# Kernel optimization log

Hardware: AMD Instinct MI355X
Metric: run time of the kernel (lower is better)

## Reference

```python
import jax, jax.numpy as jnp
import numpy as np

B, S, D, H, W1, G = 2, 4096, 768, 12, 256, 8  # W1 = one-sided window (attention_window // 2)
HD = D // H
NC = S // W1  # number of query chunks of size W1
NEG = -1e9


def setup_inputs():
    key = jax.random.key(0)
    ks = jax.random.split(key, 9)
    def w(k):
        return jax.random.normal(k, (D, D), jnp.float32) * 0.02
    zb = jnp.zeros((D,), jnp.float32)
    # mask: >0 global, 0 local, <0 masked. First G tokens are global.
    mask = jnp.zeros((B, 1, 1, S), jnp.int32).at[:, :, :, :G].set(1)
    return {
        "hidden_states": jax.random.normal(ks[0], (B, S, D), jnp.float32),
        "attention_mask": mask,
        "Wq": w(ks[1]), "bq": zb,
        "Wk": w(ks[2]), "bk": zb,
        "Wv": w(ks[3]), "bv": zb,
        "Wqg": w(ks[4]), "bqg": zb,
        "Wkg": w(ks[5]), "bkg": zb,
        "Wvg": w(ks[6]), "bvg": zb,
        "Wo": w(ks[7]), "bo": zb,
        "n_global": G,
    }


def reference(hidden_states, attention_mask, Wq, bq, Wk, bk, Wv, bv,
              Wqg, bqg, Wkg, bkg, Wvg, bvg, Wo, bo, n_global):
    g = n_global
    mask = attention_mask.reshape(B, S)
    key_neg = mask < 0  # masked-out positions
    scale = 1.0 / np.sqrt(HD)

    def heads(x):  # [B,S,D] -> [B,H,S,HD]
        return x.reshape(B, S, H, HD).transpose(0, 2, 1, 3)

    q = heads(hidden_states @ Wq + bq) * scale
    k = heads(hidden_states @ Wk + bk)
    v = heads(hidden_states @ Wv + bv)

    # ---- sliding-window (banded) scores via 3-chunk gather ----
    idx = jnp.arange(NC)[:, None] * W1 + jnp.arange(3 * W1)[None, :]  # [NC,3W] into padded seq
    k_ch = jnp.pad(k, ((0, 0), (0, 0), (W1, W1), (0, 0)))[:, :, idx]  # [B,H,NC,3W,HD]
    q_ch = q.reshape(B, H, NC, W1, HD)
    band = jnp.einsum('bhcqd,bhckd->bhcqk', q_ch, k_ch)  # [B,H,NC,W,3W]

    qi = jnp.arange(W1)
    kj = jnp.arange(3 * W1)
    band_ok = jnp.abs(kj[None, :] - W1 - qi[:, None]) <= W1        # [W,3W] |j-i|<=w
    j_abs = idx - W1                                               # absolute key index
    in_range = (j_abs >= 0) & (j_abs < S)                          # [NC,3W]
    neg_ch = jnp.pad(key_neg, ((0, 0), (W1, W1)))[:, idx]          # [B,NC,3W]
    valid = (band_ok[None, None, None]
             & in_range[None, None, :, None, :]
             & (~neg_ch)[:, None, :, None, :])                     # [B,1,NC,W,3W]
    band = jnp.where(valid, band, NEG)

    # ---- scores of every query against the global keys (regular k proj) ----
    glob = jnp.einsum('bhsd,bhgd->bhsg', q, k[:, :, :g])           # [B,H,S,G]
    glob = jnp.where(key_neg[:, None, None, :g], NEG, glob)

    scores = jnp.concatenate([glob.reshape(B, H, NC, W1, g), band], axis=-1)
    probs = jax.nn.softmax(scores, axis=-1)
    probs = jnp.where(key_neg.reshape(B, 1, NC, W1, 1), 0.0, probs)  # zero masked query rows

    v_ch = jnp.pad(v, ((0, 0), (0, 0), (W1, W1), (0, 0)))[:, :, idx]
    out = jnp.einsum('bhcqk,bhckd->bhcqd', probs[..., g:], v_ch)
    out = out + jnp.einsum('bhcqg,bhgd->bhcqd', probs[..., :g], v[:, :, :g])
    out = out.reshape(B, H, S, HD)

    # ---- global tokens: full attention with dedicated global projections ----
    qg = heads(hidden_states @ Wqg + bqg)[:, :, :g] * scale        # [B,H,G,HD]
    kg = heads(hidden_states @ Wkg + bkg)
    vg = heads(hidden_states @ Wvg + bvg)
    gs = jnp.einsum('bhgd,bhsd->bhgs', qg, kg)                     # [B,H,G,S]
    gs = jnp.where(key_neg[:, None, None, :], NEG, gs)
    gp = jax.nn.softmax(gs, axis=-1)
    og = jnp.einsum('bhgs,bhsd->bhgd', gp, vg)
    out = out.at[:, :, :g].set(og)

    merged = out.transpose(0, 2, 1, 3).reshape(B, S, D)
    return merged @ Wo + bo  # outer output projection
```

## Files before the change

### kernel.cpp

```cpp
#include <hip/hip_runtime.h>

#define BB 2
#define SS 4096
#define DD 768
#define HH 12
#define HDD 64
#define W1C 256
#define NCC 16
#define GG 8

typedef unsigned short u16;
typedef __attribute__((ext_vector_type(4))) unsigned short u16x4;
typedef __attribute__((ext_vector_type(8))) unsigned short u16x8;
typedef __attribute__((ext_vector_type(8))) short s16x8;
typedef __attribute__((ext_vector_type(4))) float f32x4;

__device__ __forceinline__ float b2f(u16 u) {
  union { unsigned int i; float f; } v;
  v.i = ((unsigned int)u) << 16;
  return v.f;
}
__device__ __forceinline__ u16 f2b(float f) {
  union { float f; unsigned int i; } v;
  v.f = f;
  unsigned int r = v.i + 0x7FFFu + ((v.i >> 16) & 1u);
  return (u16)(r >> 16);
}
__device__ __forceinline__ float fexp2(float x) {
#if __has_builtin(__builtin_amdgcn_exp2f)
  return __builtin_amdgcn_exp2f(x);
#else
  return exp2f(x);
#endif
}
__device__ __forceinline__ unsigned pk_bf16(float lo, float hi) {
  unsigned r;
  asm("v_cvt_pk_bf16_f32 %0, %1, %2" : "=v"(r) : "v"(lo), "v"(hi));
  return r;
}
__device__ __forceinline__ void load_lds16(const void* g, void* l) {
  __builtin_amdgcn_global_load_lds(
      (const __attribute__((address_space(1))) unsigned int*)g,
      (__attribute__((address_space(3))) unsigned int*)l, 16, 0, 0);
}

#define QSCALE 0.18033688011112042f

__global__ __launch_bounds__(256) void cvt_f32_bf16(
    const float* __restrict__ in, u16* __restrict__ out, int n8) {
  int i = blockIdx.x * 256 + threadIdx.x;
  if (i >= n8) return;
  const float4* p = (const float4*)(in + (size_t)i * 8);
  float4 a = p[0], b = p[1];
  u16x8 o;
  o[0] = f2b(a.x); o[1] = f2b(a.y); o[2] = f2b(a.z); o[3] = f2b(a.w);
  o[4] = f2b(b.x); o[5] = f2b(b.y); o[6] = f2b(b.z); o[7] = f2b(b.w);
  *(u16x8*)(out + (size_t)i * 8) = o;
}

struct WtArgs { const float* W[6]; };

__global__ __launch_bounds__(256) void transpose_wt(WtArgs wa,
                                                    u16* __restrict__ WT) {
  __shared__ float T[64][65];
  const int mat = blockIdx.z;
  const int k0 = blockIdx.y * 64;
  const int n0 = blockIdx.x * 64;
  const float* __restrict__ W = wa.W[mat];
  const int t = threadIdx.x;
#pragma unroll
  for (int i = 0; i < 4; i++) {
    int idx4 = t + i * 256;
    int r = idx4 >> 4, c4 = idx4 & 15;
    float4 v = *(const float4*)(W + (size_t)(k0 + r) * 768 + n0 + c4 * 4);
    T[r][c4 * 4 + 0] = v.x; T[r][c4 * 4 + 1] = v.y;
    T[r][c4 * 4 + 2] = v.z; T[r][c4 * 4 + 3] = v.w;
  }
  __syncthreads();
#pragma unroll
  for (int i = 0; i < 2; i++) {
    int ci = t + i * 256;
    int nl = ci >> 3, k8 = ci & 7;
    u16x8 o;
#pragma unroll
    for (int jj = 0; jj < 8; jj++) o[jj] = f2b(T[k8 * 8 + jj][nl]);
    *(u16x8*)(WT + ((size_t)mat * 768 + n0 + nl) * 768 + k0 + k8 * 8) = o;
  }
}

struct BiasArgs { const float* bias[5]; };

template <int MODE>
__global__ __launch_bounds__(512, 1) void gemm_bf16(
    const u16* __restrict__ A, const u16* __restrict__ WT, BiasArgs ba,
    u16* __restrict__ outb, float* __restrict__ outf) {
  constexpr int BM = (MODE == 0) ? 256 : 128;
  constexpr int WM = BM / 2;
  constexpr int MHAL = BM / 128;
  constexpr int ATILE = BM * 64 * 2;
  constexpr int BTILE = 256 * 64 * 2;
  constexpr int BUFB = ATILE + BTILE;
  constexpr int ACH = ATILE / 1024;
  constexpr int ALD = ACH / 8;
  constexpr int NTL = (MODE == 0) ? 15 : 3;
  constexpr int NWG = (MODE == 0) ? 480 : 192;
  constexpr int NT = 12;

  extern __shared__ __align__(16) char smem[];

  const int tid = threadIdx.x;
  const int w = tid >> 6, l = tid & 63;
  const int lq = l & 15, g = l >> 4;
  const int wm = w >> 2, wn = w & 3;

  const int cpx = NWG >> 3;
  const int id = (int)blockIdx.x;
  const int swz = (id & 7) * cpx + (id >> 3);
  const int bm = swz / NTL, bn = swz % NTL;
  const int m0 = bm * BM;
  const int nw0 = bn * 256;
  const int wsel = (MODE == 0) ? (bn / 3) : 0;
  const int nmat0 = (MODE == 0) ? ((bn % 3) * 256) : (bn * 256);
  const float* __restrict__ bias = ba.bias[wsel];

  f32x4 acc[MHAL * 4][4];
#pragma unroll
  for (int i = 0; i < MHAL * 4; i++)
#pragma unroll
    for (int j = 0; j < 4; j++) acc[i][j] = (f32x4){0.f, 0.f, 0.f, 0.f};

  auto stage = [&](int t) {
    const int k0 = t * 64;
    char* uA = smem + (t & 1) * BUFB;
    char* uB = uA + ATILE;
#pragma unroll
    for (int j = 0; j < ALD; j++) {
      const int ci = j * 8 + w;
      const int p = ci * 64 + l;
      const int row = p >> 3, sl = p & 7;
      load_lds16(A + (size_t)(m0 + row) * 768 + k0 + ((sl ^ (row & 7)) * 8),
                 uA + ci * 1024);
    }
#pragma unroll
    for (int j = 0; j < 4; j++) {
      const int ci = j * 8 + w;
      const int p = ci * 64 + l;
      const int row = p >> 3, sl = p & 7;
      load_lds16(WT + (size_t)(nw0 + row) * 768 + k0 + ((sl ^ (row & 7)) * 8),
                 uB + ci * 1024);
    }
  };

  stage(0);
  stage(1);
  if constexpr (MODE == 0)
    asm volatile("s_waitcnt vmcnt(8)" ::: "memory");
  else
    asm volatile("s_waitcnt vmcnt(6)" ::: "memory");
  __builtin_amdgcn_sched_barrier(0);
  __builtin_amdgcn_s_barrier();
  __builtin_amdgcn_sched_barrier(0);

  for (int kt = 0; kt < NT; kt++) {
    const int cur = kt & 1;
    const u16* rA = (const u16*)(smem + cur * BUFB);
    const u16* rB = (const u16*)(smem + cur * BUFB + ATILE);

#pragma unroll
    for (int nh = 0; nh < 2; nh++) {
      s16x8 bf[2][2];
#pragma unroll
      for (int nj = 0; nj < 2; nj++) {
        const int r = wn * 64 + (nh * 2 + nj) * 16 + lq;
#pragma unroll
        for (int ks = 0; ks < 2; ks++)
          bf[nj][ks] =
              *(const s16x8*)(rB + r * 64 + (((ks * 4 + g) ^ (r & 7)) * 8));
      }
#pragma unroll
      for (int mh = 0; mh < MHAL; mh++) {
        s16x8 af[4][2];
#pragma unroll
        for (int mi = 0; mi < 4; mi++) {
          const int r = wm * WM + (mh * 4 + mi) * 16 + lq;
#pragma unroll
          for (int ks = 0; ks < 2; ks++)
            af[mi][ks] =
                *(const s16x8*)(rA + r * 64 + (((ks * 4 + g) ^ (r & 7)) * 8));
        }
        __builtin_amdgcn_s_setprio(1);
#pragma unroll
        for (int mi = 0; mi < 4; mi++)
#pragma unroll
          for (int nj = 0; nj < 2; nj++)
#pragma unroll
            for (int ks = 0; ks < 2; ks++)
              acc[mh * 4 + mi][nh * 2 + nj] =
                  __builtin_amdgcn_mfma_f32_16x16x32_bf16(
                      af[mi][ks], bf[nj][ks], acc[mh * 4 + mi][nh * 2 + nj],
                      0, 0, 0);
        __builtin_amdgcn_s_setprio(0);
      }
    }

    asm volatile("s_waitcnt lgkmcnt(0)" ::: "memory");
    __builtin_amdgcn_sched_barrier(0);
    __builtin_amdgcn_s_barrier();
    __builtin_amdgcn_sched_barrier(0);
    if (kt < NT - 2) stage(kt + 2);
    if (kt < NT - 2) {
      if constexpr (MODE == 0)
        asm volatile("s_waitcnt vmcnt(8)" ::: "memory");
      else
        asm volatile("s_waitcnt vmcnt(6)" ::: "memory");
    } else {
      asm volatile("s_waitcnt vmcnt(0)" ::: "memory");
    }
    __builtin_amdgcn_sched_barrier(0);
    __builtin_amdgcn_s_barrier();
    __builtin_amdgcn_sched_barrier(0);
  }

  if (MODE == 0) {
    const float scale = (wsel == 0) ? QSCALE : 1.0f;
    u16* outw = outb + (size_t)wsel * ((size_t)BB * HH * SS * HDD);
#pragma unroll
    for (int nj = 0; nj < 4; nj++) {
      const int c = nmat0 + wn * 64 + nj * 16 + lq;
      const float bv = bias[c];
      const int h = c >> 6, hd = c & 63;
#pragma unroll
      for (int mi = 0; mi < MHAL * 4; mi++) {
#pragma unroll
        for (int r = 0; r < 4; r++) {
          const int m = m0 + wm * WM + mi * 16 + g * 4 + r;
          const int b = m >> 12, s = m & 4095;
          outw[((size_t)(b * HH + h) * SS + s) * HDD + hd] =
              f2b((acc[mi][nj][r] + bv) * scale);
        }
      }
    }
  } else {
#pragma unroll
    for (int nj = 0; nj < 4; nj++) {
      const int c = nmat0 + wn * 64 + nj * 16 + lq;
      const float bv = bias[c];
#pragma unroll
      for (int mi = 0; mi < MHAL * 4; mi++) {
#pragma unroll
        for (int r = 0; r < 4; r++) {
          const int m = m0 + wm * WM + mi * 16 + g * 4 + r;
          outf[(size_t)m * 768 + c] = acc[mi][nj][r] + bv;
        }
      }
    }
  }
}

__global__ __launch_bounds__(256) void qg_proj(
    const float* __restrict__ hs, const float* __restrict__ Wqg,
    const float* __restrict__ bqg, u16* __restrict__ QG) {
  __shared__ float hsL[8][768];
  const int bh = blockIdx.x;
  const int b = bh / HH, h = bh % HH;
  const int t = threadIdx.x;
#pragma unroll
  for (int i = 0; i < 6; i++) {
    int idx = t + i * 256;
    int row = idx / 192, c4 = idx % 192;
    *(float4*)&hsL[row][c4 * 4] =
        *(const float4*)(hs + ((size_t)b * SS + row) * DD + c4 * 4);
  }
  __syncthreads();
#pragma unroll
  for (int rep = 0; rep < 2; rep++) {
    int qi = rep * 4 + (t >> 6);
    int d = t & 63, n = h * 64 + d;
    float acc = bqg[n];
    for (int k = 0; k < DD; k++)
      acc = fmaf(hsL[qi][k], Wqg[(size_t)k * DD + n], acc);
    QG[((size_t)bh * 16 + qi) * 64 + d] = f2b(acc * QSCALE);
  }
#pragma unroll
  for (int i = 0; i < 2; i++) {
    int idx = t + i * 256;
    int row = 8 + (idx >> 6), d = idx & 63;
    QG[((size_t)bh * 16 + row) * 64 + d] = 0;
  }
}

template <int GLOBAL>
__global__ __launch_bounds__(256) void attn_mfma(
    const u16* __restrict__ Q, const u16* __restrict__ K,
    const u16* __restrict__ V, const int* __restrict__ amask,
    u16* __restrict__ ATT, float* __restrict__ Pnum,
    float* __restrict__ Pden) {
  extern __shared__ __align__(16) char smem[];
  const int tid = threadIdx.x;
  const int w = tid >> 6, lane = tid & 63;
  const int lq = lane & 15, g = lane >> 4;
  const int h = blockIdx.y, b = blockIdx.z;
  const int bh = b * HH + h;
  const size_t bhs = (size_t)bh * SS;
  const int q0 = GLOBAL ? 0 : (int)blockIdx.x * 64;
  const int split = GLOBAL ? (int)blockIdx.x : 0;

  char* Kl;
  char* VT;
  if constexpr (GLOBAL) {
    Kl = smem + w * 16384;
    VT = Kl + 8192;
  } else {
    Kl = smem;
    VT = smem + 8192;
  }

  s16x8 qf[2];
  {
    const u16* qp = GLOBAL ? (Q + ((size_t)bh * 16 + lq) * 64)
                           : (Q + (bhs + q0 + w * 16 + lq) * 64);
    qf[0] = *(const s16x8*)(qp + g * 8);
    qf[1] = *(const s16x8*)(qp + 32 + g * 8);
  }

  f32x4 oacc[4];
#pragma unroll
  for (int i = 0; i < 4; i++) oacc[i] = (f32x4){0.f, 0.f, 0.f, 0.f};
  float denom = 0.f;

  const int NT = GLOBAL ? 2 : 10;
  for (int kt = 0; kt < NT; kt++) {
    int j0, klimit;
    bool bandfree;
    if constexpr (GLOBAL) {
      j0 = split * 512 + (w * 2 + kt) * 64;
      bandfree = true;
      klimit = 64;
    } else {
      if (kt < 9) { j0 = q0 - 256 + kt * 64; bandfree = false; klimit = 64; }
      else        { j0 = 0;                  bandfree = true;  klimit = 8; }
    }

    int jm = j0 + lane;
    int mv = ((unsigned)jm < (unsigned)SS) ? amask[b * SS + jm] : -1;
    bool okk = (mv >= 0) && (lane < klimit);
    unsigned long long vm = __ballot(okk);

    if constexpr (GLOBAL) {
      asm volatile("s_waitcnt lgkmcnt(0)" ::: "memory");
      const u16* Ks = K + bhs * 64 + (size_t)j0 * 64;
#pragma unroll
      for (int i = 0; i < 8; i++) {
        int ci = i * 64 + lane;
        int row = ci >> 3, cc = ci & 7, cs = cc ^ (row & 7);
        load_lds16(Ks + row * 64 + cs * 8, Kl + i * 1024);
      }
      const u16* Vs = V + bhs * 64 + (size_t)j0 * 64;
#pragma unroll
      for (int p = 0; p < 8; p++) {
        u16x8 vv = *(const u16x8*)(Vs + (size_t)lane * 64 + p * 8);
#pragma unroll
        for (int e = 0; e < 8; e++)
          *(u16*)(VT + (p * 8 + e) * 128 + ((lane * 2) ^ (e << 4))) = vv[e];
      }
      asm volatile("s_waitcnt vmcnt(0) lgkmcnt(0)" ::: "memory");
    } else {
      __syncthreads();
      if (j0 >= 0 && j0 + 64 <= SS) {
        const u16* Ks = K + bhs * 64 + (size_t)j0 * 64;
#pragma unroll
        for (int i = 0; i < 2; i++) {
          int ci = (i * 4 + w) * 64 + lane;
          int row = ci >> 3, cc = ci & 7, cs = cc ^ (row & 7);
          load_lds16(Ks + row * 64 + cs * 8, Kl + (i * 4 + w) * 1024);
        }
      } else {
#pragma unroll
        for (int i = 0; i < 2; i++) {
          int ci = (i * 4 + w) * 64 + lane;
          int row = ci >> 3, cc = ci & 7, cs = cc ^ (row & 7);
          int jj = j0 + row;
          u16x8 val;
#pragma unroll
          for (int e = 0; e < 8; e++) val[e] = 0;
          if ((unsigned)jj < (unsigned)SS)
            val = *(const u16x8*)(K + (bhs + jj) * 64 + cs * 8);
          *(u16x8*)(Kl + ci * 16) = val;
        }
      }
#pragma unroll
      for (int p = 0; p < 2; p++) {
        int d0 = p * 32 + w * 8;
        int jj = j0 + lane;
        u16x8 vv;
#pragma unroll
        for (int e = 0; e < 8; e++) vv[e] = 0;
        if ((unsigned)jj < (unsigned)SS)
          vv = *(const u16x8*)(V + (bhs + jj) * 64 + d0);
#pragma unroll
        for (int e = 0; e < 8; e++)
          *(u16*)(VT + (d0 + e) * 128 + ((lane * 2) ^ (e << 4))) = vv[e];
      }
      asm volatile("s_waitcnt vmcnt(0)" ::: "memory");
      __syncthreads();
    }

    f32x4 sc[4];
#pragma unroll
    for (int i = 0; i < 4; i++) sc[i] = (f32x4){0.f, 0.f, 0.f, 0.f};
#pragma unroll
    for (int s = 0; s < 2; s++) {
#pragma unroll
      for (int ks = 0; ks < 4; ks++) {
        s16x8 kf = *(const s16x8*)(Kl + (ks * 16 + lq) * 128 +
                                   (((s * 4 + g) ^ (lq & 7)) << 4));
        sc[ks] = __builtin_amdgcn_mfma_f32_16x16x32_bf16(kf, qf[s], sc[ks],
                                                          0, 0, 0);
      }
    }

    {
      const unsigned mlo = (unsigned)vm, mhi = (unsigned)(vm >> 32);
      const int q_abs = q0 + w * 16 + lq;
      bool allin = bandfree;
      if constexpr (!GLOBAL) {
        const int qw = q0 + w * 16;
        allin = bandfree || (j0 >= qw - 241 && j0 <= qw + 193);
      }
      const bool fast = (vm == ~0ull) && allin;
      const int ddq = j0 + g * 4 - q_abs;
      const int gsh = g * 4;
      if (fast) {
#pragma unroll
        for (int ks = 0; ks < 4; ks++)
#pragma unroll
          for (int r = 0; r < 4; r++) {
            float p = fexp2(sc[ks][r]);
            sc[ks][r] = p;
            denom += p;
          }
      } else {
#pragma unroll
        for (int ks = 0; ks < 4; ks++)
#pragma unroll
          for (int r = 0; r < 4; r++) {
            float e = fexp2(sc[ks][r]);
            unsigned bit =
                ((ks < 2 ? mlo : mhi) >> (gsh + ((ks & 1) * 16 + r))) & 1u;
            bool ok = bit && (allin ||
                              (unsigned)(ddq + ks * 16 + r + 256) <= 512u);
            float p = ok ? e : 0.f;
            sc[ks][r] = p;
            denom += p;
          }
      }
    }

#pragma unroll
    for (int s = 0; s < 2; s++) {
      const int srcA = lq + ((g & 1) << 5);
      const bool hiSel = g >= 2;
      float L[4], H[4];
#pragma unroll
      for (int r = 0; r < 4; r++) {
        float a0 = __shfl(sc[2 * s][r], srcA);
        float a1 = __shfl(sc[2 * s + 1][r], srcA);
        L[r] = hiSel ? a1 : a0;
        float b0 = __shfl(sc[2 * s][r], srcA + 16);
        float b1 = __shfl(sc[2 * s + 1][r], srcA + 16);
        H[r] = hiSel ? b1 : b0;
      }
      union { unsigned u[4]; s16x8 v; } pf;
      pf.u[0] = pk_bf16(L[0], L[1]);
      pf.u[1] = pk_bf16(L[2], L[3]);
      pf.u[2] = pk_bf16(H[0], H[1]);
      pf.u[3] = pk_bf16(H[2], H[3]);
#pragma unroll
      for (int dblk = 0; dblk < 4; dblk++) {
        s16x8 vf = *(const s16x8*)(VT + (dblk * 16 + lq) * 128 +
                                   (((s * 4 + g) ^ (lq & 7)) << 4));
        oacc[dblk] = __builtin_amdgcn_mfma_f32_16x16x32_bf16(vf, pf.v,
                                                              oacc[dblk],
                                                              0, 0, 0);
      }
    }
  }

  denom += __shfl_xor(denom, 16);
  denom += __shfl_xor(denom, 32);
  if constexpr (!GLOBAL) {
    const int q_abs = q0 + w * 16 + lq;
    const float rowscale = (amask[b * SS + q_abs] >= 0) ? (1.f / denom) : 0.f;
    u16* orow = ATT + ((size_t)b * SS + q_abs) * DD + h * 64;
#pragma unroll
    for (int dblk = 0; dblk < 4; dblk++) {
      u16x4 o;
#pragma unroll
      for (int r = 0; r < 4; r++) o[r] = f2b(oacc[dblk][r] * rowscale);
      *(u16x4*)(orow + dblk * 16 + g * 4) = o;
    }
  } else {
    const int pidx = split * 4 + w;
    float* np = Pnum + ((size_t)bh * 32 + pidx) * 1024;
#pragma unroll
    for (int dblk = 0; dblk < 4; dblk++)
#pragma unroll
      for (int r = 0; r < 4; r++)
        np[(dblk * 16 + g * 4 + r) * 16 + lq] = oacc[dblk][r];
    Pden[((size_t)bh * 32 + pidx) * 16 + lq] = denom;
  }
}

__global__ __launch_bounds__(512) void gmerge(const float* __restrict__ Pnum,
                                              const float* __restrict__ Pden,
                                              u16* __restrict__ ATT) {
  const int bh = blockIdx.x;
  const int b = bh / HH, h = bh % HH;
  const int t = threadIdx.x;
  const int q = t >> 6, d = t & 63;
  float num = 0.f, den = 0.f;
#pragma unroll 4
  for (int p = 0; p < 32; p++) {
    num += Pnum[((size_t)bh * 32 + p) * 1024 + d * 16 + q];
    den += Pden[((size_t)bh * 32 + p) * 16 + q];
  }
  ATT[((size_t)b * SS + q) * DD + h * 64 + d] = f2b(num / den);
}

extern "C" void kernel_launch(void* const* d_in, const int* in_sizes, int n_in,
                              void* d_out, int out_size, void* d_ws,
                              size_t ws_size, hipStream_t stream) {
  const float* hs = (const float*)d_in[0];
  const int* amask = (const int*)d_in[1];
  const float* Wq = (const float*)d_in[2];
  const float* bq = (const float*)d_in[3];
  const float* Wk = (const float*)d_in[4];
  const float* bk = (const float*)d_in[5];
  const float* Wv = (const float*)d_in[6];
  const float* bv = (const float*)d_in[7];
  const float* Wqg = (const float*)d_in[8];
  const float* bqg = (const float*)d_in[9];
  const float* Wkg = (const float*)d_in[10];
  const float* bkg = (const float*)d_in[11];
  const float* Wvg = (const float*)d_in[12];
  const float* bvg = (const float*)d_in[13];
  const float* Wo = (const float*)d_in[14];
  const float* bo = (const float*)d_in[15];
  float* out = (float*)d_out;

  char* ws = (char*)d_ws;
  const size_t QSZB = (size_t)BB * HH * SS * HDD * 2;
  u16* Qb = (u16*)(ws + 0);
  u16* Kb = (u16*)(ws + QSZB);
  u16* Vb = (u16*)(ws + 2 * QSZB);
  u16* KGb = (u16*)(ws + 3 * QSZB);
  u16* VGb = (u16*)(ws + 4 * QSZB);
  u16* Ab = (u16*)(ws + 5 * QSZB);
  u16* WTb = (u16*)(ws + 6 * QSZB);
  u16* ATTb = (u16*)(ws + 6 * QSZB + 7077888);
  u16* QGb = (u16*)(ws + 7 * QSZB + 7077888);
  float* Pnum = (float*)(ws + 7 * QSZB + 7077888 + 49152);
  float* Pden = (float*)(ws + 7 * QSZB + 7077888 + 49152 + 3145728);

  hipLaunchKernelGGL(cvt_f32_bf16, dim3(3072), dim3(256), 0, stream, hs, Ab,
                     (int)((size_t)BB * SS * DD / 8));

  WtArgs wa;
  wa.W[0] = Wq; wa.W[1] = Wk; wa.W[2] = Wv;
  wa.W[3] = Wkg; wa.W[4] = Wvg; wa.W[5] = Wo;
  hipLaunchKernelGGL(transpose_wt, dim3(12, 12, 6), dim3(256), 0, stream, wa,
                     WTb);

  BiasArgs b0;
  b0.bias[0] = bq; b0.bias[1] = bk; b0.bias[2] = bv;
  b0.bias[3] = bkg; b0.bias[4] = bvg;
  hipLaunchKernelGGL((gemm_bf16<0>), dim3(480), dim3(512), 131072, stream,
                     Ab, WTb, b0, Qb, (float*)nullptr);

  hipLaunchKernelGGL(qg_proj, dim3(24), dim3(256), 0, stream, hs, Wqg, bqg,
                     QGb);

  hipLaunchKernelGGL((attn_mfma<1>), dim3(8, HH, BB), dim3(256), 65536,
                     stream, QGb, KGb, VGb, amask, (u16*)nullptr, Pnum, Pden);

  hipLaunchKernelGGL((attn_mfma<0>), dim3(64, HH, BB), dim3(256), 16384,
                     stream, Qb, Kb, Vb, amask, ATTb, (float*)nullptr,
                     (float*)nullptr);

  hipLaunchKernelGGL(gmerge, dim3(24), dim3(512), 0, stream, Pnum, Pden, ATTb);

  BiasArgs b1;
  for (int i = 0; i < 5; i++) b1.bias[i] = bo;
  hipLaunchKernelGGL((gemm_bf16<1>), dim3(192), dim3(512), 98304, stream,
                     ATTb, WTb + (size_t)5 * 768 * 768, b1, (u16*)nullptr,
                     out);
}
```

Before: 209.3 us.

## Use 128-row GEMM tiles with triple-buffered LDS and issue-ahead prefetch

The bf16 GEMM now uses a uniform 128x256 tile for both the QKV and output projections, which doubles the QKV grid to 960 workgroups. LDS goes from double to triple buffering (147 KB). The next-next tile's global-to-LDS loads are issued before the current tile's MFMAs, so one barrier per iteration suffices and loads overlap compute. The setprio hints are dropped. Smaller tiles lower per-block reuse and enlarge the grid, in exchange for better load balancing and deeper overlap.

```diff
diff --git a/kernel.cpp b/kernel.cpp
--- a/kernel.cpp
+++ b/kernel.cpp
@@ -94,17 +94,12 @@
 __global__ __launch_bounds__(512, 1) void gemm_bf16(
     const u16* __restrict__ A, const u16* __restrict__ WT, BiasArgs ba,
     u16* __restrict__ outb, float* __restrict__ outf) {
-  constexpr int BM = (MODE == 0) ? 256 : 128;
-  constexpr int WM = BM / 2;
-  constexpr int MHAL = BM / 128;
-  constexpr int ATILE = BM * 64 * 2;
-  constexpr int BTILE = 256 * 64 * 2;
-  constexpr int BUFB = ATILE + BTILE;
-  constexpr int ACH = ATILE / 1024;
-  constexpr int ALD = ACH / 8;
   constexpr int NTL = (MODE == 0) ? 15 : 3;
-  constexpr int NWG = (MODE == 0) ? 480 : 192;
+  constexpr int NWG = 64 * NTL;
   constexpr int NT = 12;
+  constexpr int ABYTES = 128 * 64 * 2;
+  constexpr int BBYTES = 256 * 64 * 2;
+  constexpr int BUFB = ABYTES + BBYTES;
 
   extern __shared__ __align__(16) char smem[];
 
@@ -117,24 +112,24 @@
   const int id = (int)blockIdx.x;
   const int swz = (id & 7) * cpx + (id >> 3);
   const int bm = swz / NTL, bn = swz % NTL;
-  const int m0 = bm * BM;
+  const int m0 = bm * 128;
   const int nw0 = bn * 256;
   const int wsel = (MODE == 0) ? (bn / 3) : 0;
   const int nmat0 = (MODE == 0) ? ((bn % 3) * 256) : (bn * 256);
   const float* __restrict__ bias = ba.bias[wsel];
 
-  f32x4 acc[MHAL * 4][4];
-#pragma unroll
-  for (int i = 0; i < MHAL * 4; i++)
+  f32x4 acc[4][4];
+#pragma unroll
+  for (int i = 0; i < 4; i++)
 #pragma unroll
     for (int j = 0; j < 4; j++) acc[i][j] = (f32x4){0.f, 0.f, 0.f, 0.f};
 
   auto stage = [&](int t) {
     const int k0 = t * 64;
-    char* uA = smem + (t & 1) * BUFB;
-    char* uB = uA + ATILE;
-#pragma unroll
-    for (int j = 0; j < ALD; j++) {
+    char* uA = smem + (t % 3) * BUFB;
+    char* uB = uA + ABYTES;
+#pragma unroll
+    for (int j = 0; j < 2; j++) {
       const int ci = j * 8 + w;
       const int p = ci * 64 + l;
       const int row = p >> 3, sl = p & 7;
@@ -153,69 +148,48 @@
 
   stage(0);
   stage(1);
-  if constexpr (MODE == 0)
-    asm volatile("s_waitcnt vmcnt(8)" ::: "memory");
-  else
-    asm volatile("s_waitcnt vmcnt(6)" ::: "memory");
+  asm volatile("s_waitcnt vmcnt(6)" ::: "memory");
   __builtin_amdgcn_sched_barrier(0);
   __builtin_amdgcn_s_barrier();
   __builtin_amdgcn_sched_barrier(0);
 
   for (int kt = 0; kt < NT; kt++) {
-    const int cur = kt & 1;
-    const u16* rA = (const u16*)(smem + cur * BUFB);
-    const u16* rB = (const u16*)(smem + cur * BUFB + ATILE);
-
-#pragma unroll
-    for (int nh = 0; nh < 2; nh++) {
-      s16x8 bf[2][2];
-#pragma unroll
-      for (int nj = 0; nj < 2; nj++) {
-        const int r = wn * 64 + (nh * 2 + nj) * 16 + lq;
+    const u16* rA = (const u16*)(smem + (kt % 3) * BUFB);
+    const u16* rB = (const u16*)(smem + (kt % 3) * BUFB + ABYTES);
+
+    if (kt < NT - 2) stage(kt + 2);
+    __builtin_amdgcn_sched_barrier(0);
+
+    s16x8 af[4][2], bf[4][2];
+#pragma unroll
+    for (int mi = 0; mi < 4; mi++) {
+      const int r = wm * 64 + mi * 16 + lq;
+#pragma unroll
+      for (int ks = 0; ks < 2; ks++)
+        af[mi][ks] =
+            *(const s16x8*)(rA + r * 64 + (((ks * 4 + g) ^ (r & 7)) * 8));
+    }
+#pragma unroll
+    for (int nj = 0; nj < 4; nj++) {
+      const int r = wn * 64 + nj * 16 + lq;
+#pragma unroll
+      for (int ks = 0; ks < 2; ks++)
+        bf[nj][ks] =
+            *(const s16x8*)(rB + r * 64 + (((ks * 4 + g) ^ (r & 7)) * 8));
+    }
+#pragma unroll
+    for (int mi = 0; mi < 4; mi++)
+#pragma unroll
+      for (int nj = 0; nj < 4; nj++)
 #pragma unroll
         for (int ks = 0; ks < 2; ks++)
-          bf[nj][ks] =
-              *(const s16x8*)(rB + r * 64 + (((ks * 4 + g) ^ (r & 7)) * 8));
-      }
-#pragma unroll
-      for (int mh = 0; mh < MHAL; mh++) {
-        s16x8 af[4][2];
-#pragma unroll
-        for (int mi = 0; mi < 4; mi++) {
-          const int r = wm * WM + (mh * 4 + mi) * 16 + lq;
-#pragma unroll
-          for (int ks = 0; ks < 2; ks++)
-            af[mi][ks] =
-                *(const s16x8*)(rA + r * 64 + (((ks * 4 + g) ^ (r & 7)) * 8));
-        }
-        __builtin_amdgcn_s_setprio(1);
-#pragma unroll
-        for (int mi = 0; mi < 4; mi++)
-#pragma unroll
-          for (int nj = 0; nj < 2; nj++)
-#pragma unroll
-            for (int ks = 0; ks < 2; ks++)
-              acc[mh * 4 + mi][nh * 2 + nj] =
-                  __builtin_amdgcn_mfma_f32_16x16x32_bf16(
-                      af[mi][ks], bf[nj][ks], acc[mh * 4 + mi][nh * 2 + nj],
-                      0, 0, 0);
-        __builtin_amdgcn_s_setprio(0);
-      }
-    }
-
-    asm volatile("s_waitcnt lgkmcnt(0)" ::: "memory");
-    __builtin_amdgcn_sched_barrier(0);
-    __builtin_amdgcn_s_barrier();
-    __builtin_amdgcn_sched_barrier(0);
-    if (kt < NT - 2) stage(kt + 2);
-    if (kt < NT - 2) {
-      if constexpr (MODE == 0)
-        asm volatile("s_waitcnt vmcnt(8)" ::: "memory");
-      else
-        asm volatile("s_waitcnt vmcnt(6)" ::: "memory");
-    } else {
+          acc[mi][nj] = __builtin_amdgcn_mfma_f32_16x16x32_bf16(
+              af[mi][ks], bf[nj][ks], acc[mi][nj], 0, 0, 0);
+
+    if (kt < NT - 2)
+      asm volatile("s_waitcnt vmcnt(6)" ::: "memory");
+    else
       asm volatile("s_waitcnt vmcnt(0)" ::: "memory");
-    }
     __builtin_amdgcn_sched_barrier(0);
     __builtin_amdgcn_s_barrier();
     __builtin_amdgcn_sched_barrier(0);
@@ -230,10 +204,10 @@
       const float bv = bias[c];
       const int h = c >> 6, hd = c & 63;
 #pragma unroll
-      for (int mi = 0; mi < MHAL * 4; mi++) {
+      for (int mi = 0; mi < 4; mi++) {
 #pragma unroll
         for (int r = 0; r < 4; r++) {
-          const int m = m0 + wm * WM + mi * 16 + g * 4 + r;
+          const int m = m0 + wm * 64 + mi * 16 + g * 4 + r;
           const int b = m >> 12, s = m & 4095;
           outw[((size_t)(b * HH + h) * SS + s) * HDD + hd] =
               f2b((acc[mi][nj][r] + bv) * scale);
@@ -246,10 +220,10 @@
       const int c = nmat0 + wn * 64 + nj * 16 + lq;
       const float bv = bias[c];
 #pragma unroll
-      for (int mi = 0; mi < MHAL * 4; mi++) {
+      for (int mi = 0; mi < 4; mi++) {
 #pragma unroll
         for (int r = 0; r < 4; r++) {
-          const int m = m0 + wm * WM + mi * 16 + g * 4 + r;
+          const int m = m0 + wm * 64 + mi * 16 + g * 4 + r;
           outf[(size_t)m * 768 + c] = acc[mi][nj][r] + bv;
         }
       }
@@ -574,7 +548,7 @@
   BiasArgs b0;
   b0.bias[0] = bq; b0.bias[1] = bk; b0.bias[2] = bv;
   b0.bias[3] = bkg; b0.bias[4] = bvg;
-  hipLaunchKernelGGL((gemm_bf16<0>), dim3(480), dim3(512), 131072, stream,
+  hipLaunchKernelGGL((gemm_bf16<0>), dim3(960), dim3(512), 147456, stream,
                      Ab, WTb, b0, Qb, (float*)nullptr);
 
   hipLaunchKernelGGL(qg_proj, dim3(24), dim3(256), 0, stream, hs, Wqg, bqg,
@@ -591,7 +565,7 @@
 
   BiasArgs b1;
   for (int i = 0; i < 5; i++) b1.bias[i] = bo;
-  hipLaunchKernelGGL((gemm_bf16<1>), dim3(192), dim3(512), 98304, stream,
+  hipLaunchKernelGGL((gemm_bf16<1>), dim3(192), dim3(512), 147456, stream,
                      ATTb, WTb + (size_t)5 * 768 * 768, b1, (u16*)nullptr,
                      out);
 }
```

Measured after the change: 203.1 us. 3.0% less time.
